# Kernel optimization log

Hardware: AMD Instinct MI355X
Metric: run time of the kernel (lower is better)

The kernel has to match this reference:

```python
import jax, jax.numpy as jnp
import numpy as np

N, E, G, F, H, L = 50000, 400000, 64, 7, 300, 100


def setup_inputs() -> dict:
    key = jax.random.key(0)
    ks = jax.random.split(key, 24)
    w = lambda k, i, o: jax.random.normal(k, (i, o), jnp.float32) * 0.05
    return {
        "x": jax.random.normal(ks[0], (N, F), jnp.float32),
        "edge_index": jax.random.randint(ks[1], (2, E), 0, N),
        "batch": jnp.sort(jax.random.randint(ks[2], (N,), 0, G)),
        "u": jax.random.normal(ks[3], (G, 2), jnp.float32),
        # EdgeLayer 0: mlp(2*F -> H -> H -> L)
        "l0_w1": w(ks[4], 2 * F, H), "l0_b1": jnp.zeros((H,), jnp.float32),
        "l0_w2": w(ks[5], H, H),     "l0_b2": jnp.zeros((H,), jnp.float32),
        "l0_w3": w(ks[6], H, L),     "l0_b3": jnp.zeros((L,), jnp.float32),
        # EdgeLayer 1: mlp(2*L -> H -> H -> L)
        "l1_w1": w(ks[7], 2 * L, H), "l1_b1": jnp.zeros((H,), jnp.float32),
        "l1_w2": w(ks[8], H, H),     "l1_b2": jnp.zeros((H,), jnp.float32),
        "l1_w3": w(ks[9], H, L),     "l1_b3": jnp.zeros((L,), jnp.float32),
        # final lin: (3*L + 2) -> L -> L -> 2
        "lin_w1": w(ks[10], 3 * L + 2, L), "lin_b1": jnp.zeros((L,), jnp.float32),
        "lin_w2": w(ks[11], L, L),          "lin_b2": jnp.zeros((L,), jnp.float32),
        "lin_w3": w(ks[12], L, 2),          "lin_b3": jnp.zeros((2,), jnp.float32),
    }


def mlp3(h, w1, b1, w2, b2, w3, b3):
    h = jax.nn.relu(h @ w1 + b1)
    h = jax.nn.relu(h @ w2 + b2)
    return h @ w3 + b3


def edge_layer(x, src, dst, w1, b1, w2, b2, w3, b3):
    # gather endpoints, per-edge MLP on [x_i, x_j - x_i], scatter-max to target nodes
    xi = x[dst]          # [E, C] target (x_i)
    xj = x[src]          # [E, C] source (x_j)
    msg = mlp3(jnp.concatenate([xi, xj - xi], axis=-1), w1, b1, w2, b2, w3, b3)
    n = x.shape[0]
    agg = jax.ops.segment_max(msg, dst, num_segments=n)
    cnt = jax.ops.segment_sum(jnp.ones((msg.shape[0], 1), msg.dtype), dst, num_segments=n)
    return jnp.where(cnt > 0, agg, 0.0)  # PyG fills empty neighborhoods with 0


def reference(x, edge_index, batch, u,
              l0_w1, l0_b1, l0_w2, l0_b2, l0_w3, l0_b3,
              l1_w1, l1_b1, l1_w2, l1_b2, l1_w3, l1_b3,
              lin_w1, lin_b1, lin_w2, lin_b2, lin_w3, lin_b3):
    src, dst = edge_index[0], edge_index[1]
    h = jax.nn.relu(edge_layer(x, src, dst, l0_w1, l0_b1, l0_w2, l0_b2, l0_w3, l0_b3))
    h = jax.nn.relu(edge_layer(h, src, dst, l1_w1, l1_b1, l1_w2, l1_b2, l1_w3, l1_b3))
    # global add / mean / max pooling per graph
    addp = jax.ops.segment_sum(h, batch, num_segments=G)
    cnt = jax.ops.segment_sum(jnp.ones((h.shape[0], 1), h.dtype), batch, num_segments=G)
    meanp = addp / jnp.maximum(cnt, 1.0)
    maxp = jax.ops.segment_max(h, batch, num_segments=G)
    maxp = jnp.where(cnt > 0, maxp, 0.0)
    pooled = jnp.concatenate([addp, meanp, maxp, u], axis=1)  # [G, 3L+2]
    return mlp3(pooled, lin_w1, lin_b1, lin_w2, lin_b2, lin_w3, lin_b3)
```

## Files before the change

### kernel.cpp

```cpp
#include <hip/hip_runtime.h>

typedef unsigned short u16;
typedef short s16x8 __attribute__((ext_vector_type(8)));
typedef float f32x4 __attribute__((ext_vector_type(4)));

#define DI __device__ __forceinline__

constexpr int N_ = 50000;
constexpr int E_ = 400000;
constexpr int G_ = 64;
constexpr int MS_ = 112;

DI u16 f2bf(float f) {
    union { unsigned u; float f; } c; c.f = f;
    unsigned u = c.u;
    u += 0x7fffu + ((u >> 16) & 1u);
    return (u16)(u >> 16);
}
DI float bf2f(u16 v) {
    union { unsigned u; float f; } c; c.u = (unsigned)v << 16;
    return c.f;
}
DI unsigned pkbf(float lo, float hi) {
    return (unsigned)f2bf(lo) | ((unsigned)f2bf(hi) << 16);
}

DI s16x8 ldv(const u16* p) { return *(const s16x8*)p; }
DI f32x4 MFMA(s16x8 a, s16x8 b, f32x4 c) {
    return __builtin_amdgcn_mfma_f32_16x16x32_bf16(a, b, c, 0, 0, 0);
}

DI s16x8 conv_frag(const f32x4 a0, const f32x4 a1, int kq, int col) {
    unsigned c0 = pkbf(fmaxf(a0[0], 0.f), fmaxf(a0[1], 0.f));
    unsigned c1 = pkbf(fmaxf(a0[2], 0.f), fmaxf(a0[3], 0.f));
    unsigned c2 = pkbf(fmaxf(a1[0], 0.f), fmaxf(a1[1], 0.f));
    unsigned c3 = pkbf(fmaxf(a1[2], 0.f), fmaxf(a1[3], 0.f));
    int aA = (kq & 1) * 128 + col * 4;
    int aB = aA + 64;
    unsigned A0 = __builtin_amdgcn_ds_bpermute(aA, (int)c0);
    unsigned A1 = __builtin_amdgcn_ds_bpermute(aA, (int)c1);
    unsigned A2 = __builtin_amdgcn_ds_bpermute(aA, (int)c2);
    unsigned A3 = __builtin_amdgcn_ds_bpermute(aA, (int)c3);
    unsigned B0 = __builtin_amdgcn_ds_bpermute(aB, (int)c0);
    unsigned B1 = __builtin_amdgcn_ds_bpermute(aB, (int)c1);
    unsigned B2 = __builtin_amdgcn_ds_bpermute(aB, (int)c2);
    unsigned B3 = __builtin_amdgcn_ds_bpermute(aB, (int)c3);
    bool hi = (kq >> 1) != 0;
    union { unsigned u[4]; s16x8 v; } o;
    o.u[0] = hi ? A2 : A0;
    o.u[1] = hi ? A3 : A1;
    o.u[2] = hi ? B2 : B0;
    o.u[3] = hi ? B3 : B1;
    return o.v;
}

__global__ __launch_bounds__(256)
void ModelGNN_35304631174019_kernel(
          const float* __restrict__ l0w1, const float* __restrict__ l0w2,
          const float* __restrict__ l0w3, const float* __restrict__ l1w1,
          const float* __restrict__ l1w2, const float* __restrict__ l1w3,
          const float* __restrict__ l0b1, const float* __restrict__ l0b2,
          const float* __restrict__ l0b3, const float* __restrict__ l1b1,
          const float* __restrict__ l1b2, const float* __restrict__ l1b3,
          float4* __restrict__ histz,
          u16* __restrict__ wt0, u16* __restrict__ wt1,
          u16* __restrict__ wt2a, u16* __restrict__ wt2b,
          u16* __restrict__ wt3a, u16* __restrict__ wt3b)
{
    int i = blockIdx.x * 256 + threadIdx.x;
    if (i < 12500) { histz[i] = make_float4(0.f, 0.f, 0.f, 0.f); return; }
    int f = i - 12500;

    if (f < 10240) {
        int sec = f >> 9, w = f & 511;
        int col = w >> 5, rem = w & 31;
        int n0c = sec >> 1, b01 = sec & 1;
        int n = n0c * 32 + b01 * 16 + col, k = rem;
        u16 v = 0;
        if (n < 300) {
            if (k < 7)                  v = f2bf(l0w1[k * 300 + n] - l0w1[(7 + k) * 300 + n]);
            else if (k >= 16 && k < 23) v = f2bf(l0w1[(7 + (k - 16)) * 300 + n]);
            else if (k == 15)           v = f2bf(l0b1[n]);
        }
        wt0[f] = v; return;
    }
    f -= 10240;
    if (f < 71680) {
        int sec = f >> 9, w = f & 511;
        int col = w >> 5, rem = w & 31;
        int n0c = sec / 14, r = sec % 14;
        int s = r >> 1, b01 = r & 1;
        int n = n0c * 32 + b01 * 16 + col, k = s * 32 + rem;
        u16 v = 0;
        if (n < 300) {
            if (k < 100)                  v = f2bf(l1w1[k * 300 + n] - l1w1[(100 + k) * 300 + n]);
            else if (k >= 112 && k < 212) v = f2bf(l1w1[(100 + (k - 112)) * 300 + n]);
            else if (k == 100)            v = f2bf(l1b1[n]);
        }
        wt1[f] = v; return;
    }
    f -= 71680;
    if (f < 204800) {
        const float* src = (f < 102400) ? l0w2 : l1w2;
        const float* bia = (f < 102400) ? l0b2 : l1b2;
        u16* dst = (f < 102400) ? wt2a : wt2b;
        int f2 = (f < 102400) ? f : f - 102400;
        int sec = f2 >> 9, w = f2 & 511;
        int col = w >> 5, rem = w & 31;
        int n0c = sec / 20, r = sec % 20;
        int s = r >> 1, b01 = r & 1;
        int n = n0c * 32 + b01 * 16 + col, k = s * 32 + rem;
        u16 v = 0;
        if (n < 300) {
            if (k < 300)       v = f2bf(src[k * 300 + n]);
            else if (k == 300) v = f2bf(bia[n]);
        }
        dst[f2] = v;
        return;
    }
    f -= 204800;
    if (f < 71680) {
        const float* src = (f < 35840) ? l0w3 : l1w3;
        const float* bia = (f < 35840) ? l0b3 : l1b3;
        u16* dst = (f < 35840) ? wt3a : wt3b;
        int f2 = (f < 35840) ? f : f - 35840;
        int sec = f2 >> 9, w = f2 & 511;
        int col = w >> 5, rem = w & 31;
        int ch = sec / 7, u = sec % 7;
        int n3 = u * 16 + col, k = ch * 32 + rem;
        u16 v = 0;
        if (n3 < 100) {
            if (k < 300)       v = f2bf(src[k * 100 + n3]);
            else if (k == 300) v = f2bf(bia[n3]);
        }
        dst[f2] = v;
        return;
    }
}

__global__ __launch_bounds__(256)
void hist_k(const int* __restrict__ ei, int* __restrict__ hist)
{
    int i = blockIdx.x * 256 + threadIdx.x;
    if (i < E_) atomicAdd(&hist[ei[E_ + i]], 1);
}

__global__ __launch_bounds__(1024)
void scan_k(int* h)
{
    __shared__ int part[1024];
    const int t = threadIdx.x;
    const int CH = 49;
    int base = t * CH;
    int end = base + CH; if (end > 50000) end = 50000;
    int s = 0;
    for (int i = base; i < end; ++i) s += h[i];
    part[t] = s;
    __syncthreads();
    for (int d = 1; d < 1024; d <<= 1) {
        int v = (t >= d) ? part[t - d] : 0;
        __syncthreads();
        part[t] += v;
        __syncthreads();
    }
    int run = (t ? part[t - 1] : 0);
    for (int i = base; i < end; ++i) { int c = h[i]; h[i] = run; run += c; }
}

__global__ __launch_bounds__(256)
void fill_k(const int* __restrict__ ei, int* __restrict__ pos, int* __restrict__ sei)
{
    int i = blockIdx.x * 256 + threadIdx.x;
    if (i >= E_) return;
    int s = ei[i], d = ei[E_ + i];
    int p = atomicAdd(&pos[d], 1);
    sei[p] = s; sei[E_ + p] = d;
}

#define COMPUTE1(WR, T2) {                                                    \
    f32x4 z_ = {0.f, 0.f, 0.f, 0.f};                                          \
    f32x4 ac_[2][2] = {{z_, z_}, {z_, z_}};                                   \
    _Pragma("unroll")                                                         \
    for (int s_ = 0; s_ < KA; ++s_) {                                         \
        _Pragma("unroll")                                                     \
        for (int rt_ = 0; rt_ < 2; ++rt_) {                                   \
            ac_[0][rt_] = MFMA(WR[2 * s_],     aF[rt_][s_], ac_[0][rt_]);     \
            ac_[1][rt_] = MFMA(WR[2 * s_ + 1], aF[rt_][s_], ac_[1][rt_]);     \
        }                                                                     \
    }                                                                         \
    _Pragma("unroll")                                                         \
    for (int rt_ = 0; rt_ < 2; ++rt_)                                         \
        a2[rt_][T2] = conv_frag(ac_[0][rt_], ac_[1][rt_], kq, col);           \
}

#define COMPUTE2(W2R, W3R, CH) {                                              \
    f32x4 z_ = {0.f, 0.f, 0.f, 0.f};                                          \
    f32x4 ac_[2][2] = {{z_, z_}, {z_, z_}};                                   \
    _Pragma("unroll")                                                         \
    for (int s_ = 0; s_ < 10; ++s_) {                                         \
        _Pragma("unroll")                                                     \
        for (int rt_ = 0; rt_ < 2; ++rt_) {                                   \
            ac_[0][rt_] = MFMA(W2R[2 * s_],     a2[rt_][s_], ac_[0][rt_]);    \
            ac_[1][rt_] = MFMA(W2R[2 * s_ + 1], a2[rt_][s_], ac_[1][rt_]);    \
        }                                                                     \
    }                                                                         \
    s16x8 a3_[2];                                                             \
    _Pragma("unroll")                                                         \
    for (int rt_ = 0; rt_ < 2; ++rt_)                                         \
        a3_[rt_] = conv_frag(ac_[0][rt_], ac_[1][rt_], kq, col);              \
    if ((CH) == 9 && kq == 1) {                                               \
        a3_[0][4] = (short)0x3f80;                                            \
        a3_[1][4] = (short)0x3f80;                                            \
    }                                                                         \
    _Pragma("unroll")                                                         \
    for (int u_ = 0; u_ < 7; ++u_) {                                          \
        mac[0][u_] = MFMA(W3R[u_], a3_[0], mac[0][u_]);                       \
        mac[1][u_] = MFMA(W3R[u_], a3_[1], mac[1][u_]);                       \
    }                                                                         \
}

template<bool FIRST>
__global__ __launch_bounds__(256, 1)
void edge_mlp(const float* __restrict__ X, const float* __restrict__ H0,
              const int* __restrict__ ei,
              const u16* __restrict__ W1, const u16* __restrict__ W2,
              const u16* __restrict__ W3,
              u16* __restrict__ msg)
{
    constexpr int KP = FIRST ? 32 : 224;
    constexpr int KA = KP / 32;
    __shared__ __align__(16) u16 SCR[4 * 32 * MS_];

    const int tid  = threadIdx.x;
    const int wave = tid >> 6, lane = tid & 63;
    const int col  = lane & 15, kq = lane >> 4;
    const int ebase = blockIdx.x * 128 + wave * 32;
    const int fragoff = col * 32 + kq * 8;

    u16* SCw = SCR + wave * (32 * MS_);

    s16x8 aF[2][KA];
    if constexpr (FIRST) {
        for (int s = lane; s < 32 * 32; s += 64) {
            int e = s >> 5, k = s & 31;
            u16 v = 0;
            if (k < 7)                  v = f2bf(X[(size_t)ei[E_ + ebase + e] * 7 + k]);
            else if (k >= 16 && k < 23) v = f2bf(X[(size_t)ei[ebase + e] * 7 + (k - 16)]);
            else if (k == 15)           v = 0x3f80;
            SCw[e * 40 + k] = v;
        }
        #pragma unroll
        for (int rt = 0; rt < 2; ++rt)
            aF[rt][0] = ldv(SCw + (rt * 16 + col) * 40 + kq * 8);
    } else {
        #pragma unroll
        for (int rt = 0; rt < 2; ++rt) {
            const int dn = ei[E_ + ebase + rt * 16 + col];
            const int sn = ei[ebase + rt * 16 + col];
            float4 lo[KA], hi[KA];
            #pragma unroll
            for (int s = 0; s < KA; ++s) {
                int b = s * 4 + kq;
                int node = (b < 14) ? dn : sn;
                int c = ((b < 14) ? b : b - 14) * 8;
                const float* r2 = H0 + (size_t)node * 100 + c;
                lo[s] = (c < 104) ? *(const float4*)r2
                                  : make_float4(0.f, 0.f, 0.f, 0.f);
                hi[s] = (c < 96)  ? *(const float4*)(r2 + 4)
                                  : make_float4(0.f, 0.f, 0.f, 0.f);
            }
            #pragma unroll
            for (int s = 0; s < KA; ++s) {
                s16x8 t;
                t[0] = (short)f2bf(lo[s].x); t[1] = (short)f2bf(lo[s].y);
                t[2] = (short)f2bf(lo[s].z); t[3] = (short)f2bf(lo[s].w);
                t[4] = (short)f2bf(hi[s].x); t[5] = (short)f2bf(hi[s].y);
                t[6] = (short)f2bf(hi[s].z); t[7] = (short)f2bf(hi[s].w);
                if (s == 3 && kq == 0) t[4] = (short)0x3f80;
                aF[rt][s] = t;
            }
        }
    }

    s16x8 a2[2][10];
    if constexpr (FIRST) {
        s16x8 wall[20];
        #pragma unroll
        for (int s = 0; s < 20; ++s) wall[s] = ldv(W1 + s * 512 + fragoff);
        #pragma unroll
        for (int t2 = 0; t2 < 10; ++t2) {
            f32x4 z = {0.f, 0.f, 0.f, 0.f};
            f32x4 ac[2][2] = {{z, z}, {z, z}};
            #pragma unroll
            for (int rt = 0; rt < 2; ++rt) {
                ac[0][rt] = MFMA(wall[2 * t2],     aF[rt][0], ac[0][rt]);
                ac[1][rt] = MFMA(wall[2 * t2 + 1], aF[rt][0], ac[1][rt]);
            }
            #pragma unroll
            for (int rt = 0; rt < 2; ++rt)
                a2[rt][t2] = conv_frag(ac[0][rt], ac[1][rt], kq, col);
        }
    } else {
        s16x8 wA[2 * KA], wB[2 * KA];
        #pragma unroll
        for (int s = 0; s < 2 * KA; ++s) wA[s] = ldv(W1 + s * 512 + fragoff);
        #pragma unroll 1
        for (int t2 = 0; t2 < 10; t2 += 2) {
            #pragma unroll
            for (int s = 0; s < 2 * KA; ++s)
                wB[s] = ldv(W1 + (size_t)(t2 + 1) * 14 * 512 + s * 512 + fragoff);
            COMPUTE1(wA, t2);
            if (t2 + 2 < 10) {
                #pragma unroll
                for (int s = 0; s < 2 * KA; ++s)
                    wA[s] = ldv(W1 + (size_t)(t2 + 2) * 14 * 512 + s * 512 + fragoff);
            }
            COMPUTE1(wB, t2 + 1);
        }
    }
    if (kq == 1) {
        a2[0][9][4] = (short)0x3f80;
        a2[1][9][4] = (short)0x3f80;
    }

    f32x4 mac[2][7];
    #pragma unroll
    for (int rt = 0; rt < 2; ++rt)
        #pragma unroll
        for (int u = 0; u < 7; ++u) { f32x4 z = {0.f, 0.f, 0.f, 0.f}; mac[rt][u] = z; }

    {
        s16x8 w2A[20], w3A[7], w2B[20], w3B[7];
        #pragma unroll
        for (int s = 0; s < 20; ++s) w2A[s] = ldv(W2 + s * 512 + fragoff);
        #pragma unroll
        for (int u = 0; u < 7; ++u)  w3A[u] = ldv(W3 + u * 512 + fragoff);
        #pragma unroll 1
        for (int ch = 0; ch < 10; ch += 2) {
            #pragma unroll
            for (int s = 0; s < 20; ++s)
                w2B[s] = ldv(W2 + (size_t)(ch + 1) * 20 * 512 + s * 512 + fragoff);
            #pragma unroll
            for (int u = 0; u < 7; ++u)
                w3B[u] = ldv(W3 + (size_t)(ch + 1) * 7 * 512 + u * 512 + fragoff);
            COMPUTE2(w2A, w3A, ch);
            if (ch + 2 < 10) {
                #pragma unroll
                for (int s = 0; s < 20; ++s)
                    w2A[s] = ldv(W2 + (size_t)(ch + 2) * 20 * 512 + s * 512 + fragoff);
                #pragma unroll
                for (int u = 0; u < 7; ++u)
                    w3A[u] = ldv(W3 + (size_t)(ch + 2) * 7 * 512 + u * 512 + fragoff);
            }
            COMPUTE2(w2B, w3B, ch + 1);
        }
    }

    #pragma unroll
    for (int rt = 0; rt < 2; ++rt) {
        const int row = rt * 16 + col;
        #pragma unroll
        for (int u = 0; u < 7; ++u) {
            unsigned p0 = pkbf(fmaxf(mac[rt][u][0], 0.f), fmaxf(mac[rt][u][1], 0.f));
            unsigned p1 = pkbf(fmaxf(mac[rt][u][2], 0.f), fmaxf(mac[rt][u][3], 0.f));
            int chb = u * 16 + kq * 4;
            *(unsigned*)(SCw + row * MS_ + chb)     = p0;
            *(unsigned*)(SCw + row * MS_ + chb + 2) = p1;
        }
    }
    u16* gdst = msg + (size_t)ebase * MS_;
    #pragma unroll
    for (int q2 = 0; q2 < 7; ++q2) {
        s16x8 v = ldv(SCw + q2 * 512 + lane * 8);
        *(s16x8*)(gdst + q2 * 512 + lane * 8) = v;
    }
}

__global__ __launch_bounds__(256)
void reduce_k(const u16* __restrict__ msg, const int* __restrict__ pos,
              float* __restrict__ agg)
{
    const int n = blockIdx.x * 4 + (threadIdx.x >> 6);
    if (n >= N_) return;
    const int lane = threadIdx.x & 63;
    const int start = n ? pos[n - 1] : 0;
    const int end   = pos[n];
    float m0 = 0.f, m1 = 0.f;
    for (int e = start; e < end; ++e) {
        const u16* row = msg + (size_t)e * MS_;
        m0 = fmaxf(m0, bf2f(row[lane]));
        if (lane < 36) m1 = fmaxf(m1, bf2f(row[64 + lane]));
    }
    agg[(size_t)n * 100 + lane] = m0;
    if (lane < 36) agg[(size_t)n * 100 + 64 + lane] = m1;
}

__global__ __launch_bounds__(256)
void pool(const float* __restrict__ agg1, const int* __restrict__ batch,
          const float* __restrict__ u, float* __restrict__ pooled)
{
    const int g = blockIdx.x;
    int lo = 0, hi = N_;
    while (lo < hi) { int mid = (lo + hi) >> 1; if (batch[mid] < g) lo = mid + 1; else hi = mid; }
    const int start = lo;
    int lo2 = start, hi2 = N_;
    while (lo2 < hi2) { int mid = (lo2 + hi2) >> 1; if (batch[mid] < g + 1) lo2 = mid + 1; else hi2 = mid; }
    const int end = lo2;

    const int c = threadIdx.x & 127, half = threadIdx.x >> 7;
    float sm = 0.f, mx = 0.f;
    if (c < 100)
        for (int n = start + half; n < end; n += 2) {
            float v = agg1[(size_t)n * 100 + c];
            sm += v; mx = fmaxf(mx, v);
        }
    __shared__ float ssum[128], smax[128];
    if (half) { ssum[c] = sm; smax[c] = mx; }
    __syncthreads();
    if (!half && c < 100) {
        sm += ssum[c]; mx = fmaxf(mx, smax[c]);
        int cnt = end - start;
        pooled[g * 302 + c]       = sm;
        pooled[g * 302 + 100 + c] = sm / fmaxf((float)cnt, 1.f);
        pooled[g * 302 + 200 + c] = mx;
    }
    if (threadIdx.x == 0) {
        pooled[g * 302 + 300] = u[g * 2];
        pooled[g * 302 + 301] = u[g * 2 + 1];
    }
}

__global__ __launch_bounds__(128)
void final_mlp(const float* __restrict__ pooled,
               const float* __restrict__ w1, const float* __restrict__ b1,
               const float* __restrict__ w2, const float* __restrict__ b2,
               const float* __restrict__ w3, const float* __restrict__ b3,
               float* __restrict__ out)
{
    const int g = blockIdx.x, t = threadIdx.x;
    __shared__ float P[302], T1[100], T2[100];
    for (int i = t; i < 302; i += 128) P[i] = pooled[g * 302 + i];
    __syncthreads();
    if (t < 100) {
        float a = b1[t];
        for (int i = 0; i < 302; ++i) a = fmaf(P[i], w1[i * 100 + t], a);
        T1[t] = fmaxf(a, 0.f);
    }
    __syncthreads();
    if (t < 100) {
        float a = b2[t];
        for (int i = 0; i < 100; ++i) a = fmaf(T1[i], w2[i * 100 + t], a);
        T2[t] = fmaxf(a, 0.f);
    }
    __syncthreads();
    if (t < 2) {
        float a = b3[t];
        for (int i = 0; i < 100; ++i) a = fmaf(T2[i], w3[i * 2 + t], a);
        out[g * 2 + t] = a;
    }
}

extern "C" void kernel_launch(void* const* d_in, const int* in_sizes, int n_in,
                              void* d_out, int out_size, void* d_ws, size_t ws_size,
                              hipStream_t stream)
{
    const float* x     = (const float*)d_in[0];
    const int*   ei    = (const int*)d_in[1];
    const int*   batch = (const int*)d_in[2];
    const float* uu    = (const float*)d_in[3];
    const float *l0w1 = (const float*)d_in[4],  *l0b1 = (const float*)d_in[5];
    const float *l0w2 = (const float*)d_in[6],  *l0b2 = (const float*)d_in[7];
    const float *l0w3 = (const float*)d_in[8],  *l0b3 = (const float*)d_in[9];
    const float *l1w1 = (const float*)d_in[10], *l1b1 = (const float*)d_in[11];
    const float *l1w2 = (const float*)d_in[12], *l1b2 = (const float*)d_in[13];
    const float *l1w3 = (const float*)d_in[14], *l1b3 = (const float*)d_in[15];
    const float *lw1  = (const float*)d_in[16], *lb1  = (const float*)d_in[17];
    const float *lw2  = (const float*)d_in[18], *lb2  = (const float*)d_in[19];
    const float *lw3  = (const float*)d_in[20], *lb3  = (const float*)d_in[21];

    char* w = (char*)d_ws;
    float* agg0   = (float*)(w);
    float* agg1   = (float*)(w + 20000000);
    float* pooled = (float*)(w + 40000000);
    u16* wt0  = (u16*)(w + 40077312);
    u16* wt1  = (u16*)(w + 40097792);
    u16* wt2a = (u16*)(w + 40241152);
    u16* wt2b = (u16*)(w + 40445952);
    u16* wt3a = (u16*)(w + 40650752);
    u16* wt3b = (u16*)(w + 40722432);
    int* hist = (int*)(w + 40794112);
    int* sei  = (int*)(w + 40994112);
    u16* msg  = (u16*)(w + 44194112);

    ModelGNN_35304631174019_kernel<<<1449, 256, 0, stream>>>(
        l0w1, l0w2, l0w3, l1w1, l1w2, l1w3,
        l0b1, l0b2, l0b3, l1b1, l1b2, l1b3,
        (float4*)hist, wt0, wt1, wt2a, wt2b, wt3a, wt3b);
    hist_k<<<1563, 256, 0, stream>>>(ei, hist);
    scan_k<<<1, 1024, 0, stream>>>(hist);
    fill_k<<<1563, 256, 0, stream>>>(ei, hist, sei);
    edge_mlp<true ><<<3125, 256, 0, stream>>>(x, nullptr, sei, wt0, wt2a, wt3a, msg);
    reduce_k<<<12500, 256, 0, stream>>>(msg, hist, agg0);
    edge_mlp<false><<<3125, 256, 0, stream>>>(nullptr, agg0, sei, wt1, wt2b, wt3b, msg);
    reduce_k<<<12500, 256, 0, stream>>>(msg, hist, agg1);
    pool<<<G_, 256, 0, stream>>>(agg1, batch, uu, pooled);
    final_mlp<<<G_, 128, 0, stream>>>(pooled, lw1, lb1, lw2, lb2, lw3, lb3, (float*)d_out);
}
```

Baseline: 1.259 ms.

## Factor first edge-MLP layer into per-node U/V GEMMs gathered per edge

The first linear layer of each edge MLP is linear in [x_i, x_j - x_i], so it is split into a per-node term U = x(W_a - W_b) + b and a per-node term V = x W_b. These are computed once per node by a new gemm_uv kernel into a 608-wide fp32 buffer. The edge kernel then gathers U[dst] + V[src] and applies relu, instead of running the first GEMM per edge. This cuts the layer-1 FLOPs by the edge/node ratio, at the cost of gathering two 300-float rows per edge and an extra kernel launch with a large intermediate buffer.

```diff
diff --git a/kernel.cpp b/kernel.cpp
--- a/kernel.cpp
+++ b/kernel.cpp
@@ -10,6 +10,7 @@
 constexpr int E_ = 400000;
 constexpr int G_ = 64;
 constexpr int MS_ = 112;
+constexpr int UVS_ = 608;
 
 DI u16 f2bf(float f) {
     union { unsigned u; float f; } c; c.f = f;
@@ -63,7 +64,7 @@
           const float* __restrict__ l0b3, const float* __restrict__ l1b1,
           const float* __restrict__ l1b2, const float* __restrict__ l1b3,
           float4* __restrict__ histz,
-          u16* __restrict__ wt0, u16* __restrict__ wt1,
+          u16* __restrict__ wtu0, u16* __restrict__ wtu1,
           u16* __restrict__ wt2a, u16* __restrict__ wt2b,
           u16* __restrict__ wt3a, u16* __restrict__ wt3b)
 {
@@ -71,35 +72,38 @@
     if (i < 12500) { histz[i] = make_float4(0.f, 0.f, 0.f, 0.f); return; }
     int f = i - 12500;
 
-    if (f < 10240) {
+    if (f < 19456) {
         int sec = f >> 9, w = f & 511;
-        int col = w >> 5, rem = w & 31;
-        int n0c = sec >> 1, b01 = sec & 1;
-        int n = n0c * 32 + b01 * 16 + col, k = rem;
+        int col = w >> 5, kq = (w & 31) >> 3, j = w & 7;
+        int chunk = sec >> 1, b01 = sec & 1;
+        int n = chunk * 32 + b01 * 16 + col;
+        int k = kq * 8 + j;
         u16 v = 0;
-        if (n < 300) {
-            if (k < 7)                  v = f2bf(l0w1[k * 300 + n] - l0w1[(7 + k) * 300 + n]);
-            else if (k >= 16 && k < 23) v = f2bf(l0w1[(7 + (k - 16)) * 300 + n]);
-            else if (k == 15)           v = f2bf(l0b1[n]);
-        }
-        wt0[f] = v; return;
-    }
-    f -= 10240;
-    if (f < 71680) {
+        if (k < 7) {
+            if (n < 300)                  v = f2bf(l0w1[k * 300 + n] - l0w1[(7 + k) * 300 + n]);
+            else if (n >= 304 && n < 604) v = f2bf(l0w1[(7 + k) * 300 + (n - 304)]);
+        } else if (k == 7) {
+            if (n < 300) v = f2bf(l0b1[n]);
+        }
+        wtu0[f] = v; return;
+    }
+    f -= 19456;
+    if (f < 77824) {
         int sec = f >> 9, w = f & 511;
-        int col = w >> 5, rem = w & 31;
-        int n0c = sec / 14, r = sec % 14;
-        int s = r >> 1, b01 = r & 1;
-        int n = n0c * 32 + b01 * 16 + col, k = s * 32 + rem;
+        int col = w >> 5, kq = (w & 31) >> 3, j = w & 7;
+        int chunk = sec >> 3, r = sec & 7, s = r >> 1, b01 = r & 1;
+        int n = chunk * 32 + b01 * 16 + col;
+        int k = s * 32 + kq * 8 + j;
         u16 v = 0;
-        if (n < 300) {
-            if (k < 100)                  v = f2bf(l1w1[k * 300 + n] - l1w1[(100 + k) * 300 + n]);
-            else if (k >= 112 && k < 212) v = f2bf(l1w1[(100 + (k - 112)) * 300 + n]);
-            else if (k == 100)            v = f2bf(l1b1[n]);
-        }
-        wt1[f] = v; return;
-    }
-    f -= 71680;
+        if (k < 100) {
+            if (n < 300)                  v = f2bf(l1w1[k * 300 + n] - l1w1[(100 + k) * 300 + n]);
+            else if (n >= 304 && n < 604) v = f2bf(l1w1[(100 + k) * 300 + (n - 304)]);
+        } else if (k == 100) {
+            if (n < 300) v = f2bf(l1b1[n]);
+        }
+        wtu1[f] = v; return;
+    }
+    f -= 77824;
     if (f < 204800) {
         const float* src = (f < 102400) ? l0w2 : l1w2;
         const float* bia = (f < 102400) ? l0b2 : l1b2;
@@ -177,20 +181,87 @@
     sei[p] = s; sei[E_ + p] = d;
 }
 
-#define COMPUTE1(WR, T2) {                                                    \
-    f32x4 z_ = {0.f, 0.f, 0.f, 0.f};                                          \
-    f32x4 ac_[2][2] = {{z_, z_}, {z_, z_}};                                   \
-    _Pragma("unroll")                                                         \
-    for (int s_ = 0; s_ < KA; ++s_) {                                         \
-        _Pragma("unroll")                                                     \
-        for (int rt_ = 0; rt_ < 2; ++rt_) {                                   \
-            ac_[0][rt_] = MFMA(WR[2 * s_],     aF[rt_][s_], ac_[0][rt_]);     \
-            ac_[1][rt_] = MFMA(WR[2 * s_ + 1], aF[rt_][s_], ac_[1][rt_]);     \
-        }                                                                     \
-    }                                                                         \
-    _Pragma("unroll")                                                         \
-    for (int rt_ = 0; rt_ < 2; ++rt_)                                         \
-        a2[rt_][T2] = conv_frag(ac_[0][rt_], ac_[1][rt_], kq, col);           \
+template<int KA>
+__global__ __launch_bounds__(256, 2)
+void gemm_uv(const float* __restrict__ A, const u16* __restrict__ W,
+             float* __restrict__ UV)
+{
+    __shared__ __align__(16) float SC[4][1024];
+    const int tid = threadIdx.x, wave = tid >> 6, lane = tid & 63;
+    const int col = lane & 15, kq = lane >> 4;
+    const int nb = blockIdx.x * 128 + wave * 32;
+    const int fragoff = col * 32 + kq * 8;
+
+    s16x8 aF[2][KA];
+    #pragma unroll
+    for (int rt = 0; rt < 2; ++rt) {
+        int node = nb + rt * 16 + col; if (node >= N_) node = N_ - 1;
+        if constexpr (KA == 1) {
+            s16x8 t = {0, 0, 0, 0, 0, 0, 0, 0};
+            if (kq == 0) {
+                const float* r = A + (size_t)node * 7;
+                #pragma unroll
+                for (int j = 0; j < 7; ++j) t[j] = (short)f2bf(r[j]);
+                t[7] = (short)0x3f80;
+            }
+            aF[rt][0] = t;
+        } else {
+            const float* r = A + (size_t)node * 100;
+            #pragma unroll
+            for (int s = 0; s < KA; ++s) {
+                int k0 = s * 32 + kq * 8;
+                s16x8 t = {0, 0, 0, 0, 0, 0, 0, 0};
+                if (k0 + 8 <= 100) {
+                    float4 a = *(const float4*)(r + k0);
+                    float4 b = *(const float4*)(r + k0 + 4);
+                    t[0] = (short)f2bf(a.x); t[1] = (short)f2bf(a.y);
+                    t[2] = (short)f2bf(a.z); t[3] = (short)f2bf(a.w);
+                    t[4] = (short)f2bf(b.x); t[5] = (short)f2bf(b.y);
+                    t[6] = (short)f2bf(b.z); t[7] = (short)f2bf(b.w);
+                } else if (k0 == 96) {
+                    float4 a = *(const float4*)(r + 96);
+                    t[0] = (short)f2bf(a.x); t[1] = (short)f2bf(a.y);
+                    t[2] = (short)f2bf(a.z); t[3] = (short)f2bf(a.w);
+                    t[4] = (short)0x3f80;
+                }
+                aF[rt][s] = t;
+            }
+        }
+    }
+
+    float* SCw = SC[wave];
+    #pragma unroll 1
+    for (int c = 0; c < 19; ++c) {
+        const u16* w0 = W + (size_t)(c * 2 * KA) * 512 + fragoff;
+        s16x8 wb[2 * KA];
+        #pragma unroll
+        for (int t = 0; t < 2 * KA; ++t) wb[t] = ldv(w0 + t * 512);
+        f32x4 z = {0.f, 0.f, 0.f, 0.f};
+        f32x4 ac[2][2] = {{z, z}, {z, z}};
+        #pragma unroll
+        for (int s = 0; s < KA; ++s)
+            #pragma unroll
+            for (int rt = 0; rt < 2; ++rt) {
+                ac[0][rt] = MFMA(wb[2 * s],     aF[rt][s], ac[0][rt]);
+                ac[1][rt] = MFMA(wb[2 * s + 1], aF[rt][s], ac[1][rt]);
+            }
+        #pragma unroll
+        for (int cb = 0; cb < 2; ++cb)
+            #pragma unroll
+            for (int rt = 0; rt < 2; ++rt)
+                #pragma unroll
+                for (int r = 0; r < 4; ++r)
+                    SCw[(rt * 16 + col) * 32 + cb * 16 + kq * 4 + r] = ac[cb][rt][r];
+        #pragma unroll
+        for (int p = 0; p < 4; ++p) {
+            int row = p * 8 + (lane >> 3);
+            int node = nb + row;
+            if (node < N_) {
+                float4 v = *(const float4*)(SCw + row * 32 + (lane & 7) * 4);
+                *(float4*)(UV + (size_t)node * UVS_ + c * 32 + (lane & 7) * 4) = v;
+            }
+        }
+    }
 }
 
 #define COMPUTE2(W2R, W3R, CH) {                                              \
@@ -219,16 +290,11 @@
     }                                                                         \
 }
 
-template<bool FIRST>
 __global__ __launch_bounds__(256, 1)
-void edge_mlp(const float* __restrict__ X, const float* __restrict__ H0,
-              const int* __restrict__ ei,
-              const u16* __restrict__ W1, const u16* __restrict__ W2,
-              const u16* __restrict__ W3,
-              u16* __restrict__ msg)
-{
-    constexpr int KP = FIRST ? 32 : 224;
-    constexpr int KA = KP / 32;
+void edge_uv(const float* __restrict__ UV, const int* __restrict__ ei,
+             const u16* __restrict__ W2, const u16* __restrict__ W3,
+             u16* __restrict__ msg)
+{
     __shared__ __align__(16) u16 SCR[4 * 32 * MS_];
 
     const int tid  = threadIdx.x;
@@ -239,83 +305,41 @@
 
     u16* SCw = SCR + wave * (32 * MS_);
 
-    s16x8 aF[2][KA];
-    if constexpr (FIRST) {
-        for (int s = lane; s < 32 * 32; s += 64) {
-            int e = s >> 5, k = s & 31;
-            u16 v = 0;
-            if (k < 7)                  v = f2bf(X[(size_t)ei[E_ + ebase + e] * 7 + k]);
-            else if (k >= 16 && k < 23) v = f2bf(X[(size_t)ei[ebase + e] * 7 + (k - 16)]);
-            else if (k == 15)           v = 0x3f80;
-            SCw[e * 40 + k] = v;
-        }
-        #pragma unroll
-        for (int rt = 0; rt < 2; ++rt)
-            aF[rt][0] = ldv(SCw + (rt * 16 + col) * 40 + kq * 8);
-    } else {
-        #pragma unroll
-        for (int rt = 0; rt < 2; ++rt) {
-            const int dn = ei[E_ + ebase + rt * 16 + col];
-            const int sn = ei[ebase + rt * 16 + col];
-            float4 lo[KA], hi[KA];
-            #pragma unroll
-            for (int s = 0; s < KA; ++s) {
-                int b = s * 4 + kq;
-                int node = (b < 14) ? dn : sn;
-                int c = ((b < 14) ? b : b - 14) * 8;
-                const float* r2 = H0 + (size_t)node * 100 + c;
-                lo[s] = (c < 104) ? *(const float4*)r2
-                                  : make_float4(0.f, 0.f, 0.f, 0.f);
-                hi[s] = (c < 96)  ? *(const float4*)(r2 + 4)
-                                  : make_float4(0.f, 0.f, 0.f, 0.f);
-            }
-            #pragma unroll
-            for (int s = 0; s < KA; ++s) {
-                s16x8 t;
-                t[0] = (short)f2bf(lo[s].x); t[1] = (short)f2bf(lo[s].y);
-                t[2] = (short)f2bf(lo[s].z); t[3] = (short)f2bf(lo[s].w);
-                t[4] = (short)f2bf(hi[s].x); t[5] = (short)f2bf(hi[s].y);
-                t[6] = (short)f2bf(hi[s].z); t[7] = (short)f2bf(hi[s].w);
-                if (s == 3 && kq == 0) t[4] = (short)0x3f80;
-                aF[rt][s] = t;
-            }
-        }
-    }
-
     s16x8 a2[2][10];
-    if constexpr (FIRST) {
-        s16x8 wall[20];
-        #pragma unroll
-        for (int s = 0; s < 20; ++s) wall[s] = ldv(W1 + s * 512 + fragoff);
-        #pragma unroll
-        for (int t2 = 0; t2 < 10; ++t2) {
-            f32x4 z = {0.f, 0.f, 0.f, 0.f};
-            f32x4 ac[2][2] = {{z, z}, {z, z}};
-            #pragma unroll
-            for (int rt = 0; rt < 2; ++rt) {
-                ac[0][rt] = MFMA(wall[2 * t2],     aF[rt][0], ac[0][rt]);
-                ac[1][rt] = MFMA(wall[2 * t2 + 1], aF[rt][0], ac[1][rt]);
-            }
-            #pragma unroll
-            for (int rt = 0; rt < 2; ++rt)
-                a2[rt][t2] = conv_frag(ac[0][rt], ac[1][rt], kq, col);
-        }
-    } else {
-        s16x8 wA[2 * KA], wB[2 * KA];
-        #pragma unroll
-        for (int s = 0; s < 2 * KA; ++s) wA[s] = ldv(W1 + s * 512 + fragoff);
-        #pragma unroll 1
-        for (int t2 = 0; t2 < 10; t2 += 2) {
-            #pragma unroll
-            for (int s = 0; s < 2 * KA; ++s)
-                wB[s] = ldv(W1 + (size_t)(t2 + 1) * 14 * 512 + s * 512 + fragoff);
-            COMPUTE1(wA, t2);
-            if (t2 + 2 < 10) {
-                #pragma unroll
-                for (int s = 0; s < 2 * KA; ++s)
-                    wA[s] = ldv(W1 + (size_t)(t2 + 2) * 14 * 512 + s * 512 + fragoff);
-            }
-            COMPUTE1(wB, t2 + 1);
+    #pragma unroll
+    for (int rt = 0; rt < 2; ++rt) {
+        const int e = ebase + rt * 16 + col;
+        const int dn = ei[E_ + e];
+        const int sn = ei[e];
+        const float* Ud = UV + (size_t)dn * UVS_;
+        const float* Vs = UV + (size_t)sn * UVS_ + 304;
+        #pragma unroll
+        for (int h = 0; h < 2; ++h) {
+            float4 ua[5], ub[5], va[5], vb[5];
+            #pragma unroll
+            for (int q = 0; q < 5; ++q) {
+                int k0 = (h * 5 + q) * 32 + kq * 8;
+                const float4 zz = make_float4(0.f, 0.f, 0.f, 0.f);
+                bool ok = (k0 <= 296);
+                ua[q] = ok ? *(const float4*)(Ud + k0)     : zz;
+                ub[q] = ok ? *(const float4*)(Ud + k0 + 4) : zz;
+                va[q] = ok ? *(const float4*)(Vs + k0)     : zz;
+                vb[q] = ok ? *(const float4*)(Vs + k0 + 4) : zz;
+            }
+            #pragma unroll
+            for (int q = 0; q < 5; ++q) {
+                unsigned p0 = pkbf(fmaxf(ua[q].x + va[q].x, 0.f),
+                                   fmaxf(ua[q].y + va[q].y, 0.f));
+                unsigned p1 = pkbf(fmaxf(ua[q].z + va[q].z, 0.f),
+                                   fmaxf(ua[q].w + va[q].w, 0.f));
+                unsigned p2 = pkbf(fmaxf(ub[q].x + vb[q].x, 0.f),
+                                   fmaxf(ub[q].y + vb[q].y, 0.f));
+                unsigned p3 = pkbf(fmaxf(ub[q].z + vb[q].z, 0.f),
+                                   fmaxf(ub[q].w + vb[q].w, 0.f));
+                union { unsigned u[4]; s16x8 v; } o;
+                o.u[0] = p0; o.u[1] = p1; o.u[2] = p2; o.u[3] = p3;
+                a2[rt][h * 5 + q] = o.v;
+            }
         }
     }
     if (kq == 1) {
@@ -482,26 +506,29 @@
     float* agg0   = (float*)(w);
     float* agg1   = (float*)(w + 20000000);
     float* pooled = (float*)(w + 40000000);
-    u16* wt0  = (u16*)(w + 40077312);
-    u16* wt1  = (u16*)(w + 40097792);
-    u16* wt2a = (u16*)(w + 40241152);
-    u16* wt2b = (u16*)(w + 40445952);
-    u16* wt3a = (u16*)(w + 40650752);
-    u16* wt3b = (u16*)(w + 40722432);
-    int* hist = (int*)(w + 40794112);
-    int* sei  = (int*)(w + 40994112);
-    u16* msg  = (u16*)(w + 44194112);
-
-    ModelGNN_35304631174019_kernel<<<1449, 256, 0, stream>>>(
+    u16* wtu0 = (u16*)(w + 40077312);
+    u16* wtu1 = (u16*)(w + 40116224);
+    u16* wt2a = (u16*)(w + 40271872);
+    u16* wt2b = (u16*)(w + 40476672);
+    u16* wt3a = (u16*)(w + 40681472);
+    u16* wt3b = (u16*)(w + 40753152);
+    int* hist = (int*)(w + 40824832);
+    int* sei  = (int*)(w + 41024832);
+    u16* msg  = (u16*)(w + 44224832);
+    float* UV = (float*)(w + 133824832);
+
+    ModelGNN_35304631174019_kernel<<<1509, 256, 0, stream>>>(
         l0w1, l0w2, l0w3, l1w1, l1w2, l1w3,
         l0b1, l0b2, l0b3, l1b1, l1b2, l1b3,
-        (float4*)hist, wt0, wt1, wt2a, wt2b, wt3a, wt3b);
+        (float4*)hist, wtu0, wtu1, wt2a, wt2b, wt3a, wt3b);
     hist_k<<<1563, 256, 0, stream>>>(ei, hist);
     scan_k<<<1, 1024, 0, stream>>>(hist);
     fill_k<<<1563, 256, 0, stream>>>(ei, hist, sei);
-    edge_mlp<true ><<<3125, 256, 0, stream>>>(x, nullptr, sei, wt0, wt2a, wt3a, msg);
+    gemm_uv<1><<<391, 256, 0, stream>>>(x, wtu0, UV);
+    edge_uv<<<3125, 256, 0, stream>>>(UV, sei, wt2a, wt3a, msg);
     reduce_k<<<12500, 256, 0, stream>>>(msg, hist, agg0);
-    edge_mlp<false><<<3125, 256, 0, stream>>>(nullptr, agg0, sei, wt1, wt2b, wt3b, msg);
+    gemm_uv<4><<<391, 256, 0, stream>>>(agg0, wtu1, UV);
+    edge_uv<<<3125, 256, 0, stream>>>(UV, sei, wt2b, wt3b, msg);
     reduce_k<<<12500, 256, 0, stream>>>(msg, hist, agg1);
     pool<<<G_, 256, 0, stream>>>(agg1, batch, uu, pooled);
     final_mlp<<<G_, 128, 0, stream>>>(pooled, lw1, lb1, lw2, lb2, lw3, lb3, (float*)d_out);
```

Measured after the change: 1.179 ms. -6.4%, faster.
